# Optimization experiments

Hardware: AMD Instinct MI355X
Metric: run time of the kernel (lower is better)

## Reference

```python
import jax, jax.numpy as jnp
import numpy as np

C_RED = 8
BN_EPS = 1e-5
NORM_EPS = 1e-6

# pairwise upper-triangular index lists (static, matches torch buffers)
_idx_i, _idx_j = [], []
for _i in range(C_RED):
    for _j in range(_i, C_RED):
        _idx_i.append(_i)
        _idx_j.append(_j)
IDX_I = np.array(_idx_i, dtype=np.int32)
IDX_J = np.array(_idx_j, dtype=np.int32)


def setup_inputs() -> dict:
    key = jax.random.key(0)
    ks = jax.random.split(key, 8)
    B, Cin, H, W = 32, 256, 56, 56
    x = jax.random.normal(ks[0], (B, Cin, H, W), dtype=jnp.float32)
    w_reduce = jax.random.normal(ks[1], (C_RED, Cin, 1, 1), dtype=jnp.float32) * 0.05
    bn_gamma = jax.random.uniform(ks[2], (C_RED,), dtype=jnp.float32, minval=0.5, maxval=1.5)
    bn_beta = jax.random.normal(ks[3], (C_RED,), dtype=jnp.float32) * 0.1
    bn_mean = jax.random.normal(ks[4], (C_RED,), dtype=jnp.float32) * 0.1
    bn_var = jax.random.uniform(ks[5], (C_RED,), dtype=jnp.float32, minval=0.5, maxval=1.5)
    w_dw = jax.random.normal(ks[6], (C_RED, 1, 3, 3), dtype=jnp.float32) * 0.3
    scale = jax.random.uniform(ks[7], (1, C_RED, 1, 1), dtype=jnp.float32, minval=0.5, maxval=1.5)
    return {"x": x, "w_reduce": w_reduce, "bn_gamma": bn_gamma, "bn_beta": bn_beta,
            "bn_mean": bn_mean, "bn_var": bn_var, "w_dw": w_dw, "scale": scale}


def _l2norm_ch(z):
    # F.normalize(p=2, dim=1, eps=1e-6): x / max(||x||_2, eps)
    n = jnp.sqrt(jnp.sum(z * z, axis=1, keepdims=True))
    return z / jnp.maximum(n, NORM_EPS)


def reference(x, w_reduce, bn_gamma, bn_beta, bn_mean, bn_var, w_dw, scale):
    # 1x1 conv (no bias)
    z = jax.lax.conv_general_dilated(x, w_reduce, (1, 1), 'VALID',
                                     dimension_numbers=('NCHW', 'OIHW', 'NCHW'))
    # BatchNorm (inference) + ReLU
    inv = bn_gamma / jnp.sqrt(bn_var + BN_EPS)
    z = z * inv[None, :, None, None] + (bn_beta - bn_mean * inv)[None, :, None, None]
    z = jax.nn.relu(z)
    # depthwise 3x3 twist conv, padding 1, times per-channel scale
    z_twist = jax.lax.conv_general_dilated(z, w_dw, (1, 1), ((1, 1), (1, 1)),
                                           dimension_numbers=('NCHW', 'OIHW', 'NCHW'),
                                           feature_group_count=C_RED) * scale
    z_norm = _l2norm_ch(z)
    z_twist_norm = _l2norm_ch(z_twist)
    # gathered pairwise products over upper-triangular channel pairs
    interactions = jnp.take(z_norm, IDX_I, axis=1) * jnp.take(z_twist_norm, IDX_J, axis=1)
    return jnp.concatenate([z_norm, interactions], axis=1)  # [B, 8+36, H, W]
```

## Files before the change

### kernel.cpp

```cpp
#include <hip/hip_runtime.h>

#define BATCH 32
#define CIN   256
#define CR    8
#define HDIM  56
#define WDIM  56
#define HW    3136
#define COUT  44

#define TILE  128

__device__ __constant__ const int PI36[36] =
    {0,0,0,0,0,0,0,0, 1,1,1,1,1,1,1, 2,2,2,2,2,2, 3,3,3,3,3, 4,4,4,4, 5,5,5, 6,6, 7};
__device__ __constant__ const int PJ36[36] =
    {0,1,2,3,4,5,6,7, 1,2,3,4,5,6,7, 2,3,4,5,6,7, 3,4,5,6,7, 4,5,6,7, 5,6,7, 6,7, 7};

__global__ __launch_bounds__(512, 6) void k1_reduce_bn_relu(
    const float* __restrict__ x, const float* __restrict__ wr,
    const float* __restrict__ gamma, const float* __restrict__ beta,
    const float* __restrict__ mean, const float* __restrict__ var,
    float* __restrict__ z)
{
    const int tid  = threadIdx.x;
    const int lane = tid & 63;
    const int wv   = __builtin_amdgcn_readfirstlane(tid >> 6);
    const int px0  = blockIdx.x * TILE;
    const int gp   = px0 + 2 * lane;
    const int b    = gp / HW;
    const int p    = gp - b * HW;
    const int cin0 = wv * 32;

    const float* __restrict__ xq =
        x + (size_t)b * CIN * HW + (size_t)cin0 * HW + p;

    float a0[CR], a1[CR];
#pragma unroll
    for (int c = 0; c < CR; ++c) { a0[c] = 0.f; a1[c] = 0.f; }

    float2 xa[8], xb[8];
    auto loadx = [&](float2 (&arr)[8], int base) {
#pragma unroll
        for (int j = 0; j < 8; ++j)
            arr[j] = *reinterpret_cast<const float2*>(
                         xq + (size_t)(base + j) * HW);
    };
    auto consume = [&](const float2 (&arr)[8], int base) {
#pragma unroll
        for (int j = 0; j < 8; ++j) {
            const int cin = cin0 + base + j;
#pragma unroll
            for (int c = 0; c < CR; ++c) {
                const float wgt = wr[c * CIN + cin];
                a0[c] = fmaf(arr[j].x, wgt, a0[c]);
                a1[c] = fmaf(arr[j].y, wgt, a1[c]);
            }
        }
    };

    loadx(xa, 0);
    loadx(xb, 8);
    consume(xa, 0);
    loadx(xa, 16);
    consume(xb, 8);
    loadx(xb, 24);
    consume(xa, 16);
    consume(xb, 24);

    __shared__ float pacc[8][TILE][CR];
#pragma unroll
    for (int c = 0; c < CR; c += 4) {
        *reinterpret_cast<float4*>(&pacc[wv][2 * lane][c]) =
            make_float4(a0[c], a0[c + 1], a0[c + 2], a0[c + 3]);
        *reinterpret_cast<float4*>(&pacc[wv][2 * lane + 1][c]) =
            make_float4(a1[c], a1[c + 1], a1[c + 2], a1[c + 3]);
    }
    __syncthreads();

    const int c = tid & 7;
    const float inv = gamma[c] / sqrtf(var[c] + 1e-5f);
    const float sh  = beta[c] - mean[c] * inv;
#pragma unroll
    for (int v = tid; v < TILE * CR; v += 512) {
        const int px = v >> 3;
        float s = 0.f;
#pragma unroll
        for (int w = 0; w < 8; ++w) s += pacc[w][px][c];
        z[(size_t)px0 * CR + v] = fmaxf(fmaf(s, inv, sh), 0.f);
    }
}

__global__ __launch_bounds__(256) void k2_dw_norm_inter(
    const float* __restrict__ z, const float* __restrict__ wdw,
    const float* __restrict__ scale, float* __restrict__ out)
{
    const int lane = threadIdx.x & 63;
    const int wv   = __builtin_amdgcn_readfirstlane(threadIdx.x >> 6);
    const int t = blockIdx.x * 64 + lane;
    const int b = t / HW;
    const int p = t - b * HW;
    const int h = p / WDIM;
    const int w = p - h * WDIM;

    const float* __restrict__ zimg = z + (size_t)b * HW * CR;

    float4 n0[9], n1[9];
    float  mk[9];
#pragma unroll
    for (int dy = -1; dy <= 1; ++dy) {
#pragma unroll
        for (int dx = -1; dx <= 1; ++dx) {
            const int k  = (dy + 1) * 3 + (dx + 1);
            const int hh = h + dy, ww = w + dx;
            const bool ok = (hh >= 0) & (hh < HDIM) & (ww >= 0) & (ww < WDIM);
            const int hc = min(max(hh, 0), HDIM - 1);
            const int wc = min(max(ww, 0), WDIM - 1);
            mk[k] = ok ? 1.0f : 0.0f;
            const float* zn = zimg + (size_t)(hc * WDIM + wc) * CR;
            n0[k] = reinterpret_cast<const float4*>(zn)[0];
            n1[k] = reinterpret_cast<const float4*>(zn)[1];
        }
    }

    const float zc[CR] = {n0[4].x, n0[4].y, n0[4].z, n0[4].w,
                          n1[4].x, n1[4].y, n1[4].z, n1[4].w};

    float tw[CR];
#pragma unroll
    for (int c = 0; c < CR; ++c) tw[c] = 0.f;
#pragma unroll
    for (int k = 0; k < 9; ++k) {
        const float nv[CR] = {n0[k].x, n0[k].y, n0[k].z, n0[k].w,
                              n1[k].x, n1[k].y, n1[k].z, n1[k].w};
#pragma unroll
        for (int c = 0; c < CR; ++c)
            tw[c] = fmaf(nv[c] * mk[k], wdw[c * 9 + k], tw[c]);
    }

    float s1 = 0.f, s2 = 0.f;
#pragma unroll
    for (int c = 0; c < CR; ++c) {
        tw[c] *= scale[c];
        s1 = fmaf(zc[c], zc[c], s1);
        s2 = fmaf(tw[c], tw[c], s2);
    }
    const float r1 = 1.0f / fmaxf(sqrtf(s1), 1e-6f);
    const float r2 = 1.0f / fmaxf(sqrtf(s2), 1e-6f);

    float a[CR], tb[CR];
#pragma unroll
    for (int c = 0; c < CR; ++c) { a[c] = zc[c] * r1; tb[c] = tw[c] * r2; }

    float* op = out + (size_t)b * COUT * HW + p;
#pragma unroll
    for (int c = 0; c < COUT; ++c) {
        if ((c / 11) == wv) {
            const float val = (c < CR) ? a[c]
                                       : a[PI36[c - CR]] * tb[PJ36[c - CR]];
            op[(size_t)c * HW] = val;
        }
    }
}

extern "C" void kernel_launch(void* const* d_in, const int* in_sizes, int n_in,
                              void* d_out, int out_size, void* d_ws, size_t ws_size,
                              hipStream_t stream) {
    const float* x     = (const float*)d_in[0];
    const float* wr    = (const float*)d_in[1];
    const float* gamma = (const float*)d_in[2];
    const float* beta  = (const float*)d_in[3];
    const float* mean  = (const float*)d_in[4];
    const float* var   = (const float*)d_in[5];
    const float* wdw   = (const float*)d_in[6];
    const float* scale = (const float*)d_in[7];
    float* out = (float*)d_out;
    float* z   = (float*)d_ws;

    const int npix = BATCH * HW;
    k1_reduce_bn_relu<<<npix / TILE, 512, 0, stream>>>(x, wr, gamma, beta, mean, var, z);
    k2_dw_norm_inter<<<npix / 64, 256, 0, stream>>>(z, wdw, scale, out);
}
```

Before: 174.9 us.

## Widen reduce kernel to 4 pixels per thread with float4 loads

The 1x1 reduce kernel now processes 256 pixels per block, with each thread handling 4 consecutive pixels through float4 loads. This halves the number of blocks and reuses each weight load across 4 pixels instead of 2. The shared partial-sum buffer is transposed to a channel-major layout so the cross-wave reduction reads contiguous pixels. Writes to z become strided by 8 floats per thread, and the occupancy hint drops from 6 to 4 blocks per SM to fit the larger register footprint and LDS tile.

Measured after the change: 175.3 us. No clear change (+0.2%).

```diff
diff --git a/kernel.cpp b/kernel.cpp
--- a/kernel.cpp
+++ b/kernel.cpp
@@ -8,14 +8,14 @@
 #define HW    3136
 #define COUT  44
 
-#define TILE  128
+#define TILE  256
 
 __device__ __constant__ const int PI36[36] =
     {0,0,0,0,0,0,0,0, 1,1,1,1,1,1,1, 2,2,2,2,2,2, 3,3,3,3,3, 4,4,4,4, 5,5,5, 6,6, 7};
 __device__ __constant__ const int PJ36[36] =
     {0,1,2,3,4,5,6,7, 1,2,3,4,5,6,7, 2,3,4,5,6,7, 3,4,5,6,7, 4,5,6,7, 5,6,7, 6,7, 7};
 
-__global__ __launch_bounds__(512, 6) void k1_reduce_bn_relu(
+__global__ __launch_bounds__(512, 4) void k1_reduce_bn_relu(
     const float* __restrict__ x, const float* __restrict__ wr,
     const float* __restrict__ gamma, const float* __restrict__ beta,
     const float* __restrict__ mean, const float* __restrict__ var,
@@ -25,7 +25,7 @@
     const int lane = tid & 63;
     const int wv   = __builtin_amdgcn_readfirstlane(tid >> 6);
     const int px0  = blockIdx.x * TILE;
-    const int gp   = px0 + 2 * lane;
+    const int gp   = px0 + 4 * lane;
     const int b    = gp / HW;
     const int p    = gp - b * HW;
     const int cin0 = wv * 32;
@@ -33,59 +33,62 @@
     const float* __restrict__ xq =
         x + (size_t)b * CIN * HW + (size_t)cin0 * HW + p;
 
-    float a0[CR], a1[CR];
+    float acc[4][CR];
 #pragma unroll
-    for (int c = 0; c < CR; ++c) { a0[c] = 0.f; a1[c] = 0.f; }
+    for (int q = 0; q < 4; ++q)
+#pragma unroll
+        for (int c = 0; c < CR; ++c) acc[q][c] = 0.f;
 
-    float2 xa[8], xb[8];
-    auto loadx = [&](float2 (&arr)[8], int base) {
+    float4 xa[4], xb[4];
+    auto loadx = [&](float4 (&arr)[4], int base) {
 #pragma unroll
-        for (int j = 0; j < 8; ++j)
-            arr[j] = *reinterpret_cast<const float2*>(
+        for (int j = 0; j < 4; ++j)
+            arr[j] = *reinterpret_cast<const float4*>(
                          xq + (size_t)(base + j) * HW);
     };
-    auto consume = [&](const float2 (&arr)[8], int base) {
+    auto consume = [&](const float4 (&arr)[4], int base) {
 #pragma unroll
-        for (int j = 0; j < 8; ++j) {
+        for (int j = 0; j < 4; ++j) {
             const int cin = cin0 + base + j;
+            const float px4[4] = {arr[j].x, arr[j].y, arr[j].z, arr[j].w};
 #pragma unroll
             for (int c = 0; c < CR; ++c) {
                 const float wgt = wr[c * CIN + cin];
-                a0[c] = fmaf(arr[j].x, wgt, a0[c]);
-                a1[c] = fmaf(arr[j].y, wgt, a1[c]);
+#pragma unroll
+                for (int q = 0; q < 4; ++q)
+                    acc[q][c] = fmaf(px4[q], wgt, acc[q][c]);
             }
         }
     };
 
     loadx(xa, 0);
-    loadx(xb, 8);
-    consume(xa, 0);
-    loadx(xa, 16);
-    consume(xb, 8);
-    loadx(xb, 24);
-    consume(xa, 16);
-    consume(xb, 24);
+    loadx(xb, 4);
+#pragma unroll
+    for (int k0 = 0; k0 < 32; k0 += 8) {
+        consume(xa, k0);
+        if (k0 + 8  < 32) loadx(xa, k0 + 8);
+        consume(xb, k0 + 4);
+        if (k0 + 12 < 32) loadx(xb, k0 + 12);
+    }
 
-    __shared__ float pacc[8][TILE][CR];
+    __shared__ float pacc[8][CR][TILE];
 #pragma unroll
-    for (int c = 0; c < CR; c += 4) {
-        *reinterpret_cast<float4*>(&pacc[wv][2 * lane][c]) =
-            make_float4(a0[c], a0[c + 1], a0[c + 2], a0[c + 3]);
-        *reinterpret_cast<float4*>(&pacc[wv][2 * lane + 1][c]) =
-            make_float4(a1[c], a1[c + 1], a1[c + 2], a1[c + 3]);
-    }
+    for (int c = 0; c < CR; ++c)
+        *reinterpret_cast<float4*>(&pacc[wv][c][4 * lane]) =
+            make_float4(acc[0][c], acc[1][c], acc[2][c], acc[3][c]);
     __syncthreads();
 
-    const int c = tid & 7;
+    const int c   = tid >> 6;
+    const int pxb = tid & 63;
     const float inv = gamma[c] / sqrtf(var[c] + 1e-5f);
     const float sh  = beta[c] - mean[c] * inv;
 #pragma unroll
-    for (int v = tid; v < TILE * CR; v += 512) {
-        const int px = v >> 3;
+    for (int k = 0; k < 4; ++k) {
+        const int px = pxb + 64 * k;
         float s = 0.f;
 #pragma unroll
-        for (int w = 0; w < 8; ++w) s += pacc[w][px][c];
-        z[(size_t)px0 * CR + v] = fmaxf(fmaf(s, inv, sh), 0.f);
+        for (int w = 0; w < 8; ++w) s += pacc[w][c][px];
+        z[(size_t)(px0 + px) * CR + c] = fmaxf(fmaf(s, inv, sh), 0.f);
     }
 }
 
```
